# Kernel tuning notes

Hardware: AMD Instinct MI355X
Metric: run time of the kernel (lower is better)

The kernel has to match this reference:

```python
import jax, jax.numpy as jnp
import numpy as np

HIDDEN = 1024
FFN = 4096
NUM_EXPERTS = 8
TOKENS = 4096


def setup_inputs() -> dict:
    key = jax.random.key(0)
    k1, k2, k3, k4 = jax.random.split(key, 4)
    x = jax.random.normal(k1, (TOKENS, HIDDEN), dtype=jnp.float32)
    router_weight = jax.random.normal(k2, (HIDDEN, NUM_EXPERTS), dtype=jnp.float32) * 0.02
    w1 = jax.random.normal(k3, (HIDDEN, FFN * NUM_EXPERTS), dtype=jnp.float32) * 0.02
    w2 = jax.random.normal(k4, (FFN * NUM_EXPERTS, HIDDEN), dtype=jnp.float32) * 0.02
    return {"x": x, "router_weight": router_weight, "w1": w1, "w2": w2, "top_k": 2}


def reference(x, router_weight, w1, w2, top_k):
    T, H = x.shape
    E = router_weight.shape[1]
    F = w1.shape[1] // E

    # Router: fp32 logits -> softmax -> top-k gating (sparse gates in dense [T, E] form)
    logits = x.astype(jnp.float32) @ router_weight  # [T, E]
    probs = jax.nn.softmax(logits, axis=-1)
    top_vals, top_idx = jax.lax.top_k(probs, top_k)  # [T, k]
    gates = jnp.zeros((T, E), dtype=probs.dtype).at[
        jnp.arange(T)[:, None], top_idx
    ].set(top_vals)  # [T, E], zero for non-selected experts

    # Per-expert FFN (expert-blocked weight layout: columns [e*F:(e+1)*F])
    w1e = w1.reshape(H, E, F)          # [H, E, F]
    w2e = w2.reshape(E, F, H)          # [E, F, H]
    h = jax.nn.gelu(jnp.einsum('th,hef->etf', x, w1e), approximate=False)  # [E, T, F]
    y = jnp.einsum('etf,efh->eth', h, w2e)  # [E, T, H]

    # Combine: gate-weighted sum over experts
    out = jnp.einsum('te,eth->th', gates.astype(y.dtype), y)  # [T, H]
    return out
```

## Files before the change

kernel.cpp:

```cpp
#include <hip/hip_runtime.h>
#include <hip/hip_bf16.h>

#define T_TOKENS 4096
#define HID 1024
#define FFN_ 4096
#define NE 8
#define MAXROWS 9216
#define MAXTILES 72
#define KSPLIT2 2

typedef unsigned short u16;
typedef __bf16 bf16x8 __attribute__((ext_vector_type(8)));
typedef float f32x4 __attribute__((ext_vector_type(4)));
typedef u16 u16x8 __attribute__((ext_vector_type(8)));

__device__ __forceinline__ u16 f2bf(float f) {
  __hip_bfloat16 h = __float2bfloat16(f);
  return *reinterpret_cast<u16*>(&h);
}

__device__ __forceinline__ void gload16(const void* g, void* l) {
  __builtin_amdgcn_global_load_lds(
      (const __attribute__((address_space(1))) void*)g,
      (__attribute__((address_space(3))) void*)l, 16, 0, 0);
}

#define WAIT_VM8() asm volatile("s_waitcnt vmcnt(8)" ::: "memory")
#define WAIT_VM0() asm volatile("s_waitcnt vmcnt(0)" ::: "memory")
#define BARRIER()  asm volatile("s_barrier" ::: "memory")

__global__ __launch_bounds__(256) void router_kernel(
    const float* __restrict__ x, const float* __restrict__ rw,
    int* __restrict__ sel, float* __restrict__ gsel, u16* __restrict__ xb) {
  int token = blockIdx.x * 4 + (threadIdx.x >> 6);
  int lane = threadIdx.x & 63;
  const float* xr = x + (size_t)token * HID;
  u16* xbr = xb + (size_t)token * HID;
  float acc[8];
#pragma unroll
  for (int e = 0; e < 8; e++) acc[e] = 0.f;
  for (int h = lane; h < HID; h += 64) {
    float xv = xr[h];
    xbr[h] = f2bf(xv);
    float4 r0 = *(const float4*)(rw + h * 8);
    float4 r1 = *(const float4*)(rw + h * 8 + 4);
    acc[0] += xv * r0.x; acc[1] += xv * r0.y; acc[2] += xv * r0.z; acc[3] += xv * r0.w;
    acc[4] += xv * r1.x; acc[5] += xv * r1.y; acc[6] += xv * r1.z; acc[7] += xv * r1.w;
  }
#pragma unroll
  for (int e = 0; e < 8; e++) {
#pragma unroll
    for (int o = 32; o > 0; o >>= 1) acc[e] += __shfl_down(acc[e], o);
  }
  if (lane == 0) {
    float mx = acc[0];
#pragma unroll
    for (int e = 1; e < 8; e++) mx = fmaxf(mx, acc[e]);
    float p[8], s = 0.f;
#pragma unroll
    for (int e = 0; e < 8; e++) { p[e] = expf(acc[e] - mx); s += p[e]; }
    float v0 = -1.f; int i0 = 0;
#pragma unroll
    for (int e = 0; e < 8; e++) if (p[e] > v0) { v0 = p[e]; i0 = e; }
    float v1 = -1.f; int i1 = 0;
#pragma unroll
    for (int e = 0; e < 8; e++) if (e != i0 && p[e] > v1) { v1 = p[e]; i1 = e; }
    float inv = 1.f / s;
    sel[token * 2] = i0;     gsel[token * 2] = v0 * inv;
    sel[token * 2 + 1] = i1; gsel[token * 2 + 1] = v1 * inv;
  }
}

__global__ __launch_bounds__(256) void hist_fill_kernel(
    const int* __restrict__ sel, int* __restrict__ counts,
    int* __restrict__ perm, float* __restrict__ grow) {
  __shared__ int lc[NE];
  if (threadIdx.x < NE) lc[threadIdx.x] = 0;
  __syncthreads();
  int gid = blockIdx.x * 256 + threadIdx.x;
  if (gid < T_TOKENS * 2) atomicAdd(&lc[sel[gid]], 1);
  if (gid < MAXROWS) { perm[gid] = -1; grow[gid] = 0.f; }
  __syncthreads();
  if (threadIdx.x < NE && lc[threadIdx.x] > 0)
    atomicAdd(&counts[threadIdx.x], lc[threadIdx.x]);
}

__global__ void base_kernel(const int* __restrict__ counts, int* __restrict__ cursor,
                            int* __restrict__ tilemap) {
  if (threadIdx.x == 0) {
    int base = 0;
    for (int e = 0; e < NE; e++) {
      cursor[e] = base;
      int padded = (base + counts[e] + 127) & ~127;
      for (int t = base >> 7; t < (padded >> 7); t++) tilemap[t] = e;
      base = padded;
    }
    for (int t = base >> 7; t < MAXTILES; t++) tilemap[t] = 0;
  }
}

__global__ __launch_bounds__(256) void scatter_kernel(
    const int* __restrict__ sel, const float* __restrict__ gsel,
    int* __restrict__ cursor, int* __restrict__ perm, float* __restrict__ grow) {
  int p = blockIdx.x * 256 + threadIdx.x;
  int e = sel[p];
  int pos = atomicAdd(&cursor[e], 1);
  perm[pos] = p >> 1;
  grow[pos] = gsel[p];
}

__global__ __launch_bounds__(256) void transpose_w1(const float* __restrict__ w1, u16* __restrict__ w1t) {
  __shared__ float tile[64][65];
  int c0 = blockIdx.x * 64;
  int r0 = blockIdx.y * 64;
  int t = threadIdx.x;
  int ci = (t & 15) * 4;
  int ri = t >> 4;
#pragma unroll
  for (int rr = 0; rr < 64; rr += 16) {
    float4 v = *(const float4*)(w1 + (size_t)(r0 + ri + rr) * 32768 + c0 + ci);
    tile[ri + rr][ci] = v.x; tile[ri + rr][ci + 1] = v.y;
    tile[ri + rr][ci + 2] = v.z; tile[ri + rr][ci + 3] = v.w;
  }
  __syncthreads();
  int j = t >> 2;
  int q = t & 3;
  u16x8 o0, o1;
#pragma unroll
  for (int k = 0; k < 8; k++) o0[k] = f2bf(tile[q * 16 + k][j]);
#pragma unroll
  for (int k = 0; k < 8; k++) o1[k] = f2bf(tile[q * 16 + 8 + k][j]);
  u16* dst = w1t + (size_t)(c0 + j) * 1024 + r0 + q * 16;
  *(u16x8*)dst = o0;
  *(u16x8*)(dst + 8) = o1;
}

__global__ __launch_bounds__(256) void transpose_w2(const float* __restrict__ w2, u16* __restrict__ w2t) {
  __shared__ float tile[64][65];
  int fb = blockIdx.x;
  int h0 = blockIdx.y * 64;
  int e = fb >> 6;
  int f0 = (fb & 63) * 64;
  int t = threadIdx.x;
  int ci = (t & 15) * 4;
  int ri = t >> 4;
#pragma unroll
  for (int rr = 0; rr < 64; rr += 16) {
    float4 v = *(const float4*)(w2 + (size_t)(fb * 64 + ri + rr) * 1024 + h0 + ci);
    tile[ri + rr][ci] = v.x; tile[ri + rr][ci + 1] = v.y;
    tile[ri + rr][ci + 2] = v.z; tile[ri + rr][ci + 3] = v.w;
  }
  __syncthreads();
  int j = t >> 2;
  int q = t & 3;
  u16x8 o0, o1;
#pragma unroll
  for (int k = 0; k < 8; k++) o0[k] = f2bf(tile[q * 16 + k][j]);
#pragma unroll
  for (int k = 0; k < 8; k++) o1[k] = f2bf(tile[q * 16 + 8 + k][j]);
  u16* dst = w2t + (size_t)e * 4194304 + (size_t)(h0 + j) * 4096 + f0 + q * 16;
  *(u16x8*)dst = o0;
  *(u16x8*)(dst + 8) = o1;
}

__global__ __launch_bounds__(256) void gemm1_kernel(
    const u16* __restrict__ xb, const u16* __restrict__ w1t,
    const int* __restrict__ perm, const float* __restrict__ grow,
    const int* __restrict__ tilemap, u16* __restrict__ hbuf,
    const u16* __restrict__ zp) {
  int bid = blockIdx.x;
  int pos = bid >> 3;
  int nt = pos / 9;
  int mt = (bid & 7) * 9 + (pos - nt * 9);
  int e = tilemap[mt];
  int row0 = mt * 128;
  int t = threadIdx.x, lane = t & 63, wave = t >> 6;
  __shared__ u16 As[2][128 * 64], Bs[2][128 * 64];

  const u16* asrc[4]; int astep[4];
  const u16* bsrc[4];
#pragma unroll
  for (int i = 0; i < 4; i++) {
    int chunk = i * 256 + t, row = chunk >> 3, c = chunk & 7;
    int cs = c ^ (row & 7);
    int tok = perm[row0 + row];
    if (tok >= 0) { asrc[i] = xb + (size_t)tok * 1024 + cs * 8; astep[i] = 64; }
    else { asrc[i] = zp + cs * 8; astep[i] = 0; }
    bsrc[i] = w1t + (size_t)e * 4194304 + (size_t)(nt * 128 + row) * 1024 + cs * 8;
  }

  f32x4 acc[4][4] = {};
  int wm = (wave >> 1) * 64, wn = (wave & 1) * 64;
  int r = lane & 15, kg = lane >> 4;
  int X = (r & 7) << 4;
  int bA0 = wm * 128 + r * 128 + ((kg * 16) ^ X);
  int bA1 = wm * 128 + r * 128 + ((64 + kg * 16) ^ X);
  int bB0 = wn * 128 + r * 128 + ((kg * 16) ^ X);
  int bB1 = wn * 128 + r * 128 + ((64 + kg * 16) ^ X);

  auto stage = [&](int p) {
#pragma unroll
    for (int i = 0; i < 4; i++)
      gload16(asrc[i], (char*)&As[p][0] + i * 4096 + wave * 1024);
#pragma unroll
    for (int i = 0; i < 4; i++)
      gload16(bsrc[i], (char*)&Bs[p][0] + i * 4096 + wave * 1024);
#pragma unroll
    for (int i = 0; i < 4; i++) { asrc[i] += astep[i]; bsrc[i] += 64; }
  };
  auto compute = [&](int p) {
    const char* Ab = (const char*)&As[p][0];
    const char* Bb = (const char*)&Bs[p][0];
#pragma unroll
    for (int kk = 0; kk < 2; kk++) {
      int bA = kk ? bA1 : bA0;
      int bB = kk ? bB1 : bB0;
      bf16x8 af[4], bfr[4];
#pragma unroll
      for (int mi = 0; mi < 4; mi++)
        af[mi] = *(const bf16x8*)(Ab + bA + mi * 2048);
#pragma unroll
      for (int ni = 0; ni < 4; ni++)
        bfr[ni] = *(const bf16x8*)(Bb + bB + ni * 2048);
#pragma unroll
      for (int mi = 0; mi < 4; mi++)
#pragma unroll
        for (int ni = 0; ni < 4; ni++)
          acc[mi][ni] = __builtin_amdgcn_mfma_f32_16x16x32_bf16(af[mi], bfr[ni], acc[mi][ni], 0, 0, 0);
    }
  };

  stage(0);
  stage(1);
  for (int ks = 0; ks < 15; ks++) {
    WAIT_VM8();
    BARRIER();
    compute(ks & 1);
    BARRIER();
    if (ks < 14) stage(ks & 1);
  }
  WAIT_VM0();
  BARRIER();
  compute(1);

  float g[4][4];
#pragma unroll
  for (int mi = 0; mi < 4; mi++)
#pragma unroll
    for (int j = 0; j < 4; j++)
      g[mi][j] = grow[row0 + wm + mi * 16 + kg * 4 + j];
#pragma unroll
  for (int mi = 0; mi < 4; mi++)
#pragma unroll
    for (int ni = 0; ni < 4; ni++)
#pragma unroll
      for (int j = 0; j < 4; j++) {
        int rl = wm + mi * 16 + kg * 4 + j;
        int col = nt * 128 + wn + ni * 16 + r;
        float v = acc[mi][ni][j];
        float ge = 0.5f * v * (1.0f + erff(v * 0.7071067811865475f)) * g[mi][j];
        hbuf[(size_t)(row0 + rl) * 4096 + col] = f2bf(ge);
      }
}

__global__ __launch_bounds__(256) void gemm2_kernel(
    const u16* __restrict__ hbuf, const u16* __restrict__ w2t,
    const int* __restrict__ perm, const int* __restrict__ tilemap,
    float* __restrict__ out) {
  int bid = blockIdx.x;
  int pos = bid >> 3;
  int rem = pos / 9;
  int mt = (bid & 7) * 9 + (pos - rem * 9);
  int ksplit = rem >> 3;
  int nt = rem & 7;
  int e = tilemap[mt];
  int row0 = mt * 128;
  int t = threadIdx.x, lane = t & 63, wave = t >> 6;
  __shared__ u16 As[2][128 * 64], Bs[2][128 * 64];

  const u16* asrc[4];
  const u16* bsrc[4];
#pragma unroll
  for (int i = 0; i < 4; i++) {
    int chunk = i * 256 + t, row = chunk >> 3, c = chunk & 7;
    int cs = c ^ (row & 7);
    asrc[i] = hbuf + (size_t)(row0 + row) * 4096 + (size_t)ksplit * 2048 + cs * 8;
    bsrc[i] = w2t + (size_t)e * 4194304 + (size_t)(nt * 128 + row) * 4096 + (size_t)ksplit * 2048 + cs * 8;
  }

  f32x4 acc[4][4] = {};
  int wm = (wave >> 1) * 64, wn = (wave & 1) * 64;
  int r = lane & 15, kg = lane >> 4;
  int X = (r & 7) << 4;
  int bA0 = wm * 128 + r * 128 + ((kg * 16) ^ X);
  int bA1 = wm * 128 + r * 128 + ((64 + kg * 16) ^ X);
  int bB0 = wn * 128 + r * 128 + ((kg * 16) ^ X);
  int bB1 = wn * 128 + r * 128 + ((64 + kg * 16) ^ X);

  auto stage = [&](int p) {
#pragma unroll
    for (int i = 0; i < 4; i++)
      gload16(asrc[i], (char*)&As[p][0] + i * 4096 + wave * 1024);
#pragma unroll
    for (int i = 0; i < 4; i++)
      gload16(bsrc[i], (char*)&Bs[p][0] + i * 4096 + wave * 1024);
#pragma unroll
    for (int i = 0; i < 4; i++) { asrc[i] += 64; bsrc[i] += 64; }
  };
  auto compute = [&](int p) {
    const char* Ab = (const char*)&As[p][0];
    const char* Bb = (const char*)&Bs[p][0];
#pragma unroll
    for (int kk = 0; kk < 2; kk++) {
      int bA = kk ? bA1 : bA0;
      int bB = kk ? bB1 : bB0;
      bf16x8 af[4], bfr[4];
#pragma unroll
      for (int mi = 0; mi < 4; mi++)
        af[mi] = *(const bf16x8*)(Ab + bA + mi * 2048);
#pragma unroll
      for (int ni = 0; ni < 4; ni++)
        bfr[ni] = *(const bf16x8*)(Bb + bB + ni * 2048);
#pragma unroll
      for (int mi = 0; mi < 4; mi++)
#pragma unroll
        for (int ni = 0; ni < 4; ni++)
          acc[mi][ni] = __builtin_amdgcn_mfma_f32_16x16x32_bf16(af[mi], bfr[ni], acc[mi][ni], 0, 0, 0);
    }
  };

  stage(0);
  stage(1);
  for (int ks = 0; ks < 31; ks++) {
    WAIT_VM8();
    BARRIER();
    compute(ks & 1);
    BARRIER();
    if (ks < 30) stage(ks & 1);
  }
  WAIT_VM0();
  BARRIER();
  compute(1);

  int tok[4][4];
#pragma unroll
  for (int mi = 0; mi < 4; mi++)
#pragma unroll
    for (int j = 0; j < 4; j++)
      tok[mi][j] = perm[row0 + wm + mi * 16 + kg * 4 + j];
#pragma unroll
  for (int mi = 0; mi < 4; mi++)
#pragma unroll
    for (int ni = 0; ni < 4; ni++)
#pragma unroll
      for (int j = 0; j < 4; j++) {
        if (tok[mi][j] >= 0) {
          int col = nt * 128 + wn + ni * 16 + r;
          atomicAdd(out + (size_t)tok[mi][j] * 1024 + col, acc[mi][ni][j]);
        }
      }
}

extern "C" void kernel_launch(void* const* d_in, const int* in_sizes, int n_in,
                              void* d_out, int out_size, void* d_ws, size_t ws_size,
                              hipStream_t stream) {
  const float* x  = (const float*)d_in[0];
  const float* rw = (const float*)d_in[1];
  const float* w1 = (const float*)d_in[2];
  const float* w2 = (const float*)d_in[3];
  float* out = (float*)d_out;
  char* ws = (char*)d_ws;

  size_t off = 0;
  auto take = [&](size_t n) { char* p = ws + off; off += (n + 255) & ~255ull; return p; };
  u16* w1t   = (u16*)take(8ull * 4096 * 1024 * 2);
  u16* w2t   = (u16*)take(8ull * 4096 * 1024 * 2);
  u16* xb    = (u16*)take((size_t)T_TOKENS * HID * 2);
  u16* hbuf  = (u16*)take((size_t)MAXROWS * FFN_ * 2);
  int* sel   = (int*)take(T_TOKENS * 2 * 4);
  float* gsel = (float*)take(T_TOKENS * 2 * 4);
  int* perm  = (int*)take(MAXROWS * 4);
  float* grow = (float*)take(MAXROWS * 4);
  int* tmap  = (int*)take(MAXTILES * 4);
  int* counts = (int*)take(NE * 4);
  int* cursor = (int*)take(NE * 4);
  u16* zp    = (u16*)take(4096);

  hipMemsetAsync(zp, 0, 4096, stream);
  hipMemsetAsync(counts, 0, NE * 4, stream);
  hipMemsetAsync(out, 0, (size_t)T_TOKENS * HID * 4, stream);

  transpose_w1<<<dim3(512, 16), 256, 0, stream>>>(w1, w1t);
  transpose_w2<<<dim3(512, 16), 256, 0, stream>>>(w2, w2t);
  router_kernel<<<dim3(T_TOKENS / 4), 256, 0, stream>>>(x, rw, sel, gsel, xb);
  hist_fill_kernel<<<dim3(MAXROWS / 256), 256, 0, stream>>>(sel, counts, perm, grow);
  base_kernel<<<dim3(1), 64, 0, stream>>>(counts, cursor, tmap);
  scatter_kernel<<<dim3(T_TOKENS * 2 / 256), 256, 0, stream>>>(sel, gsel, cursor, perm, grow);
  gemm1_kernel<<<dim3(72 * 32), 256, 0, stream>>>(xb, w1t, perm, grow, tmap, hbuf, zp);
  gemm2_kernel<<<dim3(72 * 8 * KSPLIT2), 256, 0, stream>>>(hbuf, w2t, perm, tmap, out);
}
```

Measured before the change: 395.7 us.

## Replace double-buffered LDS pipeline with single buffer and raise occupancy hint

```diff
diff --git a/kernel.cpp b/kernel.cpp
--- a/kernel.cpp
+++ b/kernel.cpp
@@ -24,10 +24,6 @@
       (const __attribute__((address_space(1))) void*)g,
       (__attribute__((address_space(3))) void*)l, 16, 0, 0);
 }
-
-#define WAIT_VM8() asm volatile("s_waitcnt vmcnt(8)" ::: "memory")
-#define WAIT_VM0() asm volatile("s_waitcnt vmcnt(0)" ::: "memory")
-#define BARRIER()  asm volatile("s_barrier" ::: "memory")
 
 __global__ __launch_bounds__(256) void router_kernel(
     const float* __restrict__ x, const float* __restrict__ rw,
@@ -163,7 +159,7 @@
   *(u16x8*)(dst + 8) = o1;
 }
 
-__global__ __launch_bounds__(256) void gemm1_kernel(
+__global__ __launch_bounds__(256, 4) void gemm1_kernel(
     const u16* __restrict__ xb, const u16* __restrict__ w1t,
     const int* __restrict__ perm, const float* __restrict__ grow,
     const int* __restrict__ tilemap, u16* __restrict__ hbuf,
@@ -175,7 +171,7 @@
   int e = tilemap[mt];
   int row0 = mt * 128;
   int t = threadIdx.x, lane = t & 63, wave = t >> 6;
-  __shared__ u16 As[2][128 * 64], Bs[2][128 * 64];
+  __shared__ u16 As[128 * 64], Bs[128 * 64];
 
   const u16* asrc[4]; int astep[4];
   const u16* bsrc[4];
@@ -198,19 +194,16 @@
   int bB0 = wn * 128 + r * 128 + ((kg * 16) ^ X);
   int bB1 = wn * 128 + r * 128 + ((64 + kg * 16) ^ X);
 
-  auto stage = [&](int p) {
+  for (int ks = 0; ks < 16; ks++) {
 #pragma unroll
     for (int i = 0; i < 4; i++)
-      gload16(asrc[i], (char*)&As[p][0] + i * 4096 + wave * 1024);
+      gload16(asrc[i], (char*)As + i * 4096 + wave * 1024);
 #pragma unroll
     for (int i = 0; i < 4; i++)
-      gload16(bsrc[i], (char*)&Bs[p][0] + i * 4096 + wave * 1024);
+      gload16(bsrc[i], (char*)Bs + i * 4096 + wave * 1024);
 #pragma unroll
     for (int i = 0; i < 4; i++) { asrc[i] += astep[i]; bsrc[i] += 64; }
-  };
-  auto compute = [&](int p) {
-    const char* Ab = (const char*)&As[p][0];
-    const char* Bb = (const char*)&Bs[p][0];
+    __syncthreads();
 #pragma unroll
     for (int kk = 0; kk < 2; kk++) {
       int bA = kk ? bA1 : bA0;
@@ -218,30 +211,18 @@
       bf16x8 af[4], bfr[4];
 #pragma unroll
       for (int mi = 0; mi < 4; mi++)
-        af[mi] = *(const bf16x8*)(Ab + bA + mi * 2048);
+        af[mi] = *(const bf16x8*)((const char*)As + bA + mi * 2048);
 #pragma unroll
       for (int ni = 0; ni < 4; ni++)
-        bfr[ni] = *(const bf16x8*)(Bb + bB + ni * 2048);
+        bfr[ni] = *(const bf16x8*)((const char*)Bs + bB + ni * 2048);
 #pragma unroll
       for (int mi = 0; mi < 4; mi++)
 #pragma unroll
         for (int ni = 0; ni < 4; ni++)
           acc[mi][ni] = __builtin_amdgcn_mfma_f32_16x16x32_bf16(af[mi], bfr[ni], acc[mi][ni], 0, 0, 0);
     }
-  };
-
-  stage(0);
-  stage(1);
-  for (int ks = 0; ks < 15; ks++) {
-    WAIT_VM8();
-    BARRIER();
-    compute(ks & 1);
-    BARRIER();
-    if (ks < 14) stage(ks & 1);
-  }
-  WAIT_VM0();
-  BARRIER();
-  compute(1);
+    __syncthreads();
+  }
 
   float g[4][4];
 #pragma unroll
@@ -263,7 +244,7 @@
       }
 }
 
-__global__ __launch_bounds__(256) void gemm2_kernel(
+__global__ __launch_bounds__(256, 4) void gemm2_kernel(
     const u16* __restrict__ hbuf, const u16* __restrict__ w2t,
     const int* __restrict__ perm, const int* __restrict__ tilemap,
     float* __restrict__ out) {
@@ -276,7 +257,7 @@
   int e = tilemap[mt];
   int row0 = mt * 128;
   int t = threadIdx.x, lane = t & 63, wave = t >> 6;
-  __shared__ u16 As[2][128 * 64], Bs[2][128 * 64];
+  __shared__ u16 As[128 * 64], Bs[128 * 64];
 
   const u16* asrc[4];
   const u16* bsrc[4];
@@ -297,19 +278,16 @@
   int bB0 = wn * 128 + r * 128 + ((kg * 16) ^ X);
   int bB1 = wn * 128 + r * 128 + ((64 + kg * 16) ^ X);
 
-  auto stage = [&](int p) {
+  for (int ks = 0; ks < 32; ks++) {
 #pragma unroll
     for (int i = 0; i < 4; i++)
-      gload16(asrc[i], (char*)&As[p][0] + i * 4096 + wave * 1024);
+      gload16(asrc[i], (char*)As + i * 4096 + wave * 1024);
 #pragma unroll
     for (int i = 0; i < 4; i++)
-      gload16(bsrc[i], (char*)&Bs[p][0] + i * 4096 + wave * 1024);
+      gload16(bsrc[i], (char*)Bs + i * 4096 + wave * 1024);
 #pragma unroll
     for (int i = 0; i < 4; i++) { asrc[i] += 64; bsrc[i] += 64; }
-  };
-  auto compute = [&](int p) {
-    const char* Ab = (const char*)&As[p][0];
-    const char* Bb = (const char*)&Bs[p][0];
+    __syncthreads();
 #pragma unroll
     for (int kk = 0; kk < 2; kk++) {
       int bA = kk ? bA1 : bA0;
@@ -317,30 +295,18 @@
       bf16x8 af[4], bfr[4];
 #pragma unroll
       for (int mi = 0; mi < 4; mi++)
-        af[mi] = *(const bf16x8*)(Ab + bA + mi * 2048);
+        af[mi] = *(const bf16x8*)((const char*)As + bA + mi * 2048);
 #pragma unroll
       for (int ni = 0; ni < 4; ni++)
-        bfr[ni] = *(const bf16x8*)(Bb + bB + ni * 2048);
+        bfr[ni] = *(const bf16x8*)((const char*)Bs + bB + ni * 2048);
 #pragma unroll
       for (int mi = 0; mi < 4; mi++)
 #pragma unroll
         for (int ni = 0; ni < 4; ni++)
           acc[mi][ni] = __builtin_amdgcn_mfma_f32_16x16x32_bf16(af[mi], bfr[ni], acc[mi][ni], 0, 0, 0);
     }
-  };
-
-  stage(0);
-  stage(1);
-  for (int ks = 0; ks < 31; ks++) {
-    WAIT_VM8();
-    BARRIER();
-    compute(ks & 1);
-    BARRIER();
-    if (ks < 30) stage(ks & 1);
-  }
-  WAIT_VM0();
-  BARRIER();
-  compute(1);
+    __syncthreads();
+  }
 
   int tok[4][4];
 #pragma unroll
```

Result: slower. 509.1 us (+28.6%).
